# Kernel tuning notes

Measured on AMD Instinct MI355X. Metric: run time of the kernel, lower is better.

The kernel has to match this reference:

```python
import jax, jax.numpy as jnp
import numpy as np

NUM_HEADS = 8
DIM_HEAD_QK = 32
DIM_HEAD_V = 32
BLOCK = 8
HALO = 3
WIN = BLOCK + 2 * HALO  # 14
SCALE = DIM_HEAD_QK ** -0.5


def rel_logits_1d(q, rel_k, permute_mask):
    N, H, W, d = q.shape
    rel_size = rel_k.shape[0]
    win = (rel_size + 1) // 2
    x = jnp.einsum('nhwd,rd->nhwr', q, rel_k)
    x = x.reshape(N * H, W, rel_size)
    x = jnp.pad(x, ((0, 0), (0, 0), (0, 1))).reshape(N * H, -1)
    x = jnp.pad(x, ((0, 0), (0, rel_size - W)))
    x = x.reshape(N * H, W + 1, rel_size)[:, :W, win - 1:]
    x = jnp.broadcast_to(x.reshape(N, H, 1, W, win), (N, H, win, W, win))
    return jnp.transpose(x, permute_mask)


def pos_embed_rel(q, height_rel, width_rel):
    BH, NB, HW, d = q.shape
    qb = q.reshape(-1, BLOCK, BLOCK, d)
    rel_w = rel_logits_1d(qb, width_rel, (0, 1, 3, 2, 4))
    rel_h = rel_logits_1d(jnp.swapaxes(qb, 1, 2), height_rel, (0, 3, 1, 4, 2))
    return (rel_h + rel_w).reshape(BH, NB, HW, WIN * WIN)


def reference(x, q_weight, kv_weight, height_rel, width_rel):
    B, C, H, W = x.shape
    nhb, nwb = H // BLOCK, W // BLOCK
    nb = nhb * nwb
    # 1x1 conv projections
    q = jnp.einsum('bchw,oc->bohw', x, q_weight)
    q = q.reshape(B * NUM_HEADS, DIM_HEAD_QK, nhb, BLOCK, nwb, BLOCK)
    q = jnp.transpose(q, (0, 1, 3, 5, 2, 4)).reshape(B * NUM_HEADS, DIM_HEAD_QK, BLOCK * BLOCK, nb)
    q = jnp.swapaxes(q, 1, 3)  # (BH, nb, BLOCK*BLOCK, dhq)
    kv = jnp.einsum('bchw,oc->bohw', x, kv_weight)
    kv = jnp.pad(kv, ((0, 0), (0, 0), (HALO, HALO), (HALO, HALO)))
    # halo windows: overlapping WINxWIN patches strided by BLOCK
    h_idx = jnp.arange(nhb)[:, None] * BLOCK + jnp.arange(WIN)[None, :]
    w_idx = jnp.arange(nwb)[:, None] * BLOCK + jnp.arange(WIN)[None, :]
    kv = kv[:, :, h_idx, :][:, :, :, :, w_idx]
    kv = jnp.transpose(kv, (0, 1, 2, 4, 3, 5)).reshape(
        B * NUM_HEADS, DIM_HEAD_QK + DIM_HEAD_V, nb, WIN * WIN)
    kv = jnp.transpose(kv, (0, 2, 3, 1))
    k, v = kv[..., :DIM_HEAD_QK], kv[..., DIM_HEAD_QK:]
    attn = jnp.einsum('bnqd,bnkd->bnqk', q, k) * SCALE
    attn = attn + pos_embed_rel(q, height_rel, width_rel)
    attn = jax.nn.softmax(attn, axis=-1)
    out = jnp.einsum('bnqk,bnkd->bnqd', attn, v)
    out = jnp.swapaxes(out, 1, 3)  # (BH, dhv, BLOCK*BLOCK, nb)
    out = out.reshape(-1, BLOCK, BLOCK, nhb, nwb)
    out = jnp.transpose(out, (0, 3, 1, 4, 2)).reshape(B, NUM_HEADS * DIM_HEAD_V, H, W)
    return out


def setup_inputs() -> dict:
    key = jax.random.key(0)
    k1, k2, k3, k4, k5 = jax.random.split(key, 5)
    dim = 256
    std = dim ** -0.5
    x = jax.random.normal(k1, (8, 256, 96, 96), dtype=jnp.float32)
    q_weight = jax.random.normal(k2, (256, 256), dtype=jnp.float32) * std
    kv_weight = jax.random.normal(k3, (512, 256), dtype=jnp.float32) * std
    height_rel = jax.random.normal(k4, (2 * WIN - 1, DIM_HEAD_QK), dtype=jnp.float32) * SCALE
    width_rel = jax.random.normal(k5, (2 * WIN - 1, DIM_HEAD_QK), dtype=jnp.float32) * SCALE
    return {'x': x, 'q_weight': q_weight, 'kv_weight': kv_weight,
            'height_rel': height_rel, 'width_rel': width_rel}
```

## Files before the change

kernel.cpp:

```cpp
#include <hip/hip_runtime.h>
#include <math.h>

#define NPIX 9216
#define SCALE 0.17677669529663687f
#define LOG2E 1.4426950408889634f

typedef __attribute__((ext_vector_type(8))) short bh8;
typedef __attribute__((ext_vector_type(4))) float f4;

__device__ __forceinline__ unsigned short f2bf(float f) {
    unsigned u = __float_as_uint(f);
    u += 0x7fff + ((u >> 16) & 1);
    return (unsigned short)(u >> 16);
}
__device__ __forceinline__ void gload_lds16(const void* g, void* l) {
    __builtin_amdgcn_global_load_lds(
        (const __attribute__((address_space(1))) unsigned int*)g,
        (__attribute__((address_space(3))) unsigned int*)l, 16, 0, 0);
}

__global__ void wconv_kernel(const float* __restrict__ qw, const float* __restrict__ kvw,
                             const float* __restrict__ hrel, const float* __restrict__ wrel,
                             unsigned short* __restrict__ Wb,
                             unsigned short* __restrict__ relb) {
    int bid = blockIdx.x, tid = threadIdx.x;
    if (bid < 768) {
        float v = (bid < 256) ? qw[bid * 256 + tid] : kvw[(bid - 256) * 256 + tid];
        Wb[bid * 256 + tid] = f2bf(v);
    } else {
        int e = (bid - 768) * 256 + tid;
        int half = e >> 10, r = (e >> 5) & 31, d = e & 31;
        float v = 0.0f;
        if (r < 27) v = (half ? wrel : hrel)[r * 32 + d] * LOG2E;
        relb[half * 1024 + r * 32 + d] = f2bf(v);
    }
}

__global__ __launch_bounds__(256) void xtrans_kernel(const float* __restrict__ x,
                                                     unsigned short* __restrict__ xt) {
    int b = blockIdx.z;
    int p0 = blockIdx.x * 128, c0 = blockIdx.y * 128;
    int tid = threadIdx.x;
    __shared__ __align__(16) unsigned short ts[128 * 136];
    const float* xb = x + (size_t)b * 256 * NPIX;
    #pragma unroll
    for (int it = 0; it < 16; ++it) {
        int e = it * 256 + tid;
        int ch = e >> 5, p4 = (e & 31) * 4;
        float4 v = *(const float4*)(xb + (size_t)(c0 + ch) * NPIX + p0 + p4);
        ts[(p4 + 0) * 136 + ch] = f2bf(v.x);
        ts[(p4 + 1) * 136 + ch] = f2bf(v.y);
        ts[(p4 + 2) * 136 + ch] = f2bf(v.z);
        ts[(p4 + 3) * 136 + ch] = f2bf(v.w);
    }
    __syncthreads();
    unsigned short* xtb = xt + (size_t)b * NPIX * 256;
    #pragma unroll
    for (int it = 0; it < 8; ++it) {
        int e = it * 256 + tid;
        int p = e >> 4, ck = (e & 15) * 8;
        *(int4*)(xtb + (size_t)(p0 + p) * 256 + c0 + ck) = *(const int4*)&ts[p * 136 + ck];
    }
}

__global__ __launch_bounds__(256) void proj_kernel(const unsigned short* __restrict__ xt,
                                                   const unsigned short* __restrict__ Wb,
                                                   unsigned short* __restrict__ qb,
                                                   unsigned short* __restrict__ kvb) {
    int flat = blockIdx.x + 72 * (blockIdx.y + 6 * blockIdx.z);
    int w = (flat & 7) * 432 + (flat >> 3);
    int n0 = (w % 6) * 128;
    int m0 = ((w / 6) % 72) * 128;
    int b  = w / 432;
    int tid = threadIdx.x, lane = tid & 63, wave = tid >> 6;
    int ll = lane & 15;
    __shared__ __align__(16) char smem[34816];
    char* As = smem;
    char* Bs = smem + 16384;
    const unsigned short* xtb = xt + (size_t)b * NPIX * 256;

    f4 acc[4][4] = {};
    int wm = (wave & 1) * 64, wn = (wave >> 1) * 64;

    for (int k0 = 0; k0 < 256; k0 += 64) {
        __syncthreads();
        #pragma unroll
        for (int i = 0; i < 4; ++i) {
            int c = wave * 4 + i;
            gload_lds16(xtb + (size_t)(m0 + c * 8 + (lane >> 3)) * 256 + k0 + (lane & 7) * 8,
                        As + c * 1024);
            gload_lds16(Wb + (size_t)(n0 + c * 8 + (lane >> 3)) * 256 + k0 + (lane & 7) * 8,
                        Bs + c * 1024);
        }
        __syncthreads();
        #pragma unroll
        for (int ks = 0; ks < 2; ++ks) {
            bh8 af[4], bf[4];
            #pragma unroll
            for (int i = 0; i < 4; ++i)
                af[i] = *(const bh8*)(As + (wm + i * 16 + ll) * 128 + ks * 64 + (lane >> 4) * 16);
            #pragma unroll
            for (int j = 0; j < 4; ++j)
                bf[j] = *(const bh8*)(Bs + (wn + j * 16 + ll) * 128 + ks * 64 + (lane >> 4) * 16);
            #pragma unroll
            for (int i = 0; i < 4; ++i)
                #pragma unroll
                for (int j = 0; j < 4; ++j)
                    acc[i][j] = __builtin_amdgcn_mfma_f32_16x16x32_bf16(af[i], bf[j], acc[i][j], 0, 0, 0);
        }
    }

    __syncthreads();
    unsigned short* ts = (unsigned short*)smem;
    int q4 = (lane >> 4) * 4;
    #pragma unroll
    for (int i = 0; i < 4; ++i) {
        #pragma unroll
        for (int j = 0; j < 4; ++j) {
            int ch = wn + j * 16 + ll;
            #pragma unroll
            for (int r = 0; r < 4; ++r)
                ts[(wm + i * 16 + q4 + r) * 136 + ch] = f2bf(acc[i][j][r]);
        }
    }
    __syncthreads();
    bool isQ = (n0 < 256);
    #pragma unroll
    for (int it = 0; it < 8; ++it) {
        int e = it * 256 + tid;
        int pixl = e >> 4, ck = (e & 15) * 8;
        int4 v = *(const int4*)&ts[pixl * 136 + ck];
        int pix = m0 + pixl, ch = n0 + ck;
        if (isQ) {
            int head = ch >> 5, d = ch & 31;
            *(int4*)&qb[((size_t)(b * 8 + head) * NPIX + pix) * 32 + d] = v;
        } else {
            int c = ch - 256, head = c >> 6, dv = c & 63;
            *(int4*)&kvb[((size_t)(b * 8 + head) * NPIX + pix) * 64 + dv] = v;
        }
    }
}

__global__ __launch_bounds__(256, 4) void attn_kernel(const unsigned short* __restrict__ qbuf,
                                                      const unsigned short* __restrict__ kvbuf,
                                                      const unsigned short* __restrict__ relb,
                                                      float* __restrict__ out) {
    int flat = blockIdx.x + 144 * blockIdx.y;
    int w = (flat & 7) * 1152 + (flat >> 3);
    int nbid = w % 144, bh = w / 144;
    int b = bh >> 3, head = bh & 7;
    int hb = nbid / 12, wblk = nbid % 12;
    int r0 = hb * 8, c0 = wblk * 8;
    int tid = threadIdx.x, lane = tid & 63, wave = tid >> 6;
    int ll = lane & 15, lq = lane >> 4;
    int m0 = wave * 16;

    __shared__ __align__(16) char smem[32512];
    unsigned short* Vt = (unsigned short*)smem;
    unsigned short* Ks = (unsigned short*)(smem + 14336);
    char* strip = smem + 14336 + wave * 4352;
    float*          RhTw = (float*)strip;
    float*          Rww  = (float*)(strip + 2240);
    unsigned short* Ps   = (unsigned short*)strip;
    float*          smR  = (float*)(smem + 32256);

    const unsigned short* qb  = qbuf  + (size_t)bh * NPIX * 32;
    const unsigned short* kvb = kvbuf + (size_t)bh * NPIX * 64;

    int qp0 = m0 + ll;
    int pixq = (r0 + (qp0 >> 3)) * 96 + c0 + (qp0 & 7);
    bh8 aq = *(const bh8*)&qb[(size_t)pixq * 32 + lq * 8];

    for (int e = tid; e < 896; e += 256) {
        int kp = e >> 2, part = e & 3;
        int a = kp >> 4, b2 = kp & 15;
        int gr = r0 + a - 3, gc = c0 + b2 - 3;
        int4 v = {0, 0, 0, 0};
        if (b2 < 14 && (unsigned)gr < 96u && (unsigned)gc < 96u)
            v = *(const int4*)&kvb[(size_t)(gr * 96 + gc) * 64 + part * 8];
        *(int4*)&Ks[kp * 40 + part * 8] = v;
    }

    #pragma unroll
    for (int it = 0; it < 2; ++it) {
        int e = it * 256 + tid;
        int part = e >> 7, kp2 = e & 127;
        if (kp2 < 112) {
            int a = kp2 >> 3, b2 = (kp2 & 7) * 2;
            int gr = r0 + a - 3, gc = c0 + b2 - 3;
            int4 lo = {0, 0, 0, 0}, hi = {0, 0, 0, 0};
            bool rok = ((kp2 & 7) < 7) && ((unsigned)gr < 96u);
            if (rok && (unsigned)gc < 96u)
                lo = *(const int4*)&kvb[(size_t)(gr * 96 + gc) * 64 + 32 + part * 8];
            if (rok && (unsigned)(gc + 1) < 96u)
                hi = *(const int4*)&kvb[(size_t)(gr * 96 + gc + 1) * 64 + 32 + part * 8];
            int g = kp2 >> 2, kb = b2 & 7;
            const unsigned* lw = (const unsigned*)&lo;
            const unsigned* hw = (const unsigned*)&hi;
            #pragma unroll
            for (int jw = 0; jw < 4; ++jw) {
                unsigned l2 = lw[jw], h2 = hw[jw];
                unsigned v0 = (l2 & 0xffffu) | (h2 << 16);
                unsigned v1 = (l2 >> 16) | (h2 & 0xffff0000u);
                int d0 = part * 8 + jw * 2;
                int s0 = (((jw * 2) & 3) + part) & 3;
                int s1 = (((jw * 2 + 1) & 3) + part) & 3;
                *(unsigned*)&Vt[d0 * 224 + ((g ^ s0) * 8) + kb] = v0;
                *(unsigned*)&Vt[(d0 + 1) * 224 + ((g ^ s1) * 8) + kb] = v1;
            }
        }
    }

    __syncthreads();

    f4 zero4 = {0.f, 0.f, 0.f, 0.f};
    f4 S[14];
    #pragma unroll
    for (int t = 0; t < 14; ++t) {
        bh8 bk = *(const bh8*)&Ks[(t * 16 + ll) * 40 + lq * 8];
        S[t] = __builtin_amdgcn_mfma_f32_16x16x32_bf16(aq, bk, zero4, 0, 0, 0);
    }

    __syncthreads();

    #pragma unroll
    for (int t = 0; t < 2; ++t) {
        int r = t * 16 + ll;
        bh8 hbv = *(const bh8*)&relb[(size_t)r * 32 + lq * 8];
        bh8 wbv = *(const bh8*)&relb[1024 + (size_t)r * 32 + lq * 8];
        f4 ch = __builtin_amdgcn_mfma_f32_16x16x32_bf16(aq, hbv, zero4, 0, 0, 0);
        f4 cw = __builtin_amdgcn_mfma_f32_16x16x32_bf16(aq, wbv, zero4, 0, 0, 0);
        if (r < 28) *(f4*)&RhTw[r * 20 + lq * 4] = ch;
        if (r >= 6 && r < 27) {
            #pragma unroll
            for (int rr = 0; rr < 4; ++rr)
                Rww[(lq * 4 + rr) * 23 + (r - 6)] = cw[rr];
        }
    }

    int row0 = m0 + lq * 4;
    int h = row0 >> 3;
    bool valid = (ll < 14);
    float rw4[4];
    #pragma unroll
    for (int rr = 0; rr < 4; ++rr) {
        int row = row0 + rr;
        rw4[rr] = valid ? Rww[(lq * 4 + rr) * 23 + 7 + ll - (row & 7)] : -INFINITY;
    }
    const float SL = SCALE * LOG2E;
    float sm4[4] = {0.f, 0.f, 0.f, 0.f};
    #pragma unroll
    for (int t = 0; t < 14; ++t) {
        f4 rh = *(const f4*)&RhTw[(13 + t - h) * 20 + lq * 4];
        #pragma unroll
        for (int rr = 0; rr < 4; ++rr) {
            float lg = S[t][rr] * SL + rh[rr] + rw4[rr];
            float p = __builtin_amdgcn_exp2f(lg);
            S[t][rr] = p;
            sm4[rr] += p;
        }
    }
    #pragma unroll
    for (int rr = 0; rr < 4; ++rr) {
        sm4[rr] += __shfl_xor(sm4[rr], 1);
        sm4[rr] += __shfl_xor(sm4[rr], 2);
        sm4[rr] += __shfl_xor(sm4[rr], 4);
        sm4[rr] += __shfl_xor(sm4[rr], 8);
    }
    if (ll == 0) {
        #pragma unroll
        for (int rr = 0; rr < 4; ++rr) smR[row0 + rr] = sm4[rr];
    }

    f4 O[2] = {zero4, zero4};
    #pragma unroll
    for (int c = 0; c < 2; ++c) {
        const int nt = c ? 6 : 8;
        #pragma unroll
        for (int tl = 0; tl < 8; ++tl) {
            if (tl < nt) {
                int t = c * 8 + tl;
                int col = tl * 16 + ll;
                #pragma unroll
                for (int rr = 0; rr < 4; ++rr)
                    Ps[(lq * 4 + rr) * 136 + col] = f2bf(S[t][rr]);
            }
        }
        const int nkt = c ? 3 : 4;
        #pragma unroll
        for (int ktl = 0; ktl < 4; ++ktl) {
            if (ktl < nkt) {
                int kt = c * 4 + ktl;
                bh8 bp = *(const bh8*)&Ps[ll * 136 + ktl * 32 + lq * 8];
                #pragma unroll
                for (int mt = 0; mt < 2; ++mt) {
                    int d = mt * 16 + ll;
                    int s = ((d & 3) + ((d >> 3) & 3)) & 3;
                    bh8 av = *(const bh8*)&Vt[d * 224 + (((kt * 4 + lq) ^ s) * 8)];
                    O[mt] = __builtin_amdgcn_mfma_f32_16x16x32_bf16(av, bp, O[mt], 0, 0, 0);
                }
            }
        }
    }

    int qp = m0 + ll;
    float rs = 1.0f / smR[qp];
    int pix = (r0 + (qp >> 3)) * 96 + c0 + (qp & 7);
    float* ob = out + (size_t)(b * 256 + head * 32) * NPIX;
    #pragma unroll
    for (int mt = 0; mt < 2; ++mt) {
        #pragma unroll
        for (int rr = 0; rr < 4; ++rr) {
            int d = mt * 16 + lq * 4 + rr;
            ob[(size_t)d * NPIX + pix] = O[mt][rr] * rs;
        }
    }
}

extern "C" void kernel_launch(void* const* d_in, const int* in_sizes, int n_in,
                              void* d_out, int out_size, void* d_ws, size_t ws_size,
                              hipStream_t stream) {
    const float* x    = (const float*)d_in[0];
    const float* qw   = (const float*)d_in[1];
    const float* kvw  = (const float*)d_in[2];
    const float* hrel = (const float*)d_in[3];
    const float* wrel = (const float*)d_in[4];
    float* out = (float*)d_out;

    char* ws = (char*)d_ws;
    unsigned short* xt    = (unsigned short*)ws;
    unsigned short* Wb    = (unsigned short*)(ws + 37748736);
    unsigned short* relb  = (unsigned short*)(ws + 38141952);
    unsigned short* qbuf  = (unsigned short*)(ws + 38146048);
    unsigned short* kvbuf = (unsigned short*)(ws + 75894784);

    wconv_kernel<<<dim3(776), 256, 0, stream>>>(qw, kvw, hrel, wrel, Wb, relb);
    xtrans_kernel<<<dim3(72, 2, 8), 256, 0, stream>>>(x, xt);
    proj_kernel<<<dim3(72, 6, 8), 256, 0, stream>>>(xt, Wb, qbuf, kvbuf);
    attn_kernel<<<dim3(144, 64), 256, 0, stream>>>(qbuf, kvbuf, relb, out);
}
```

Before: 258.5 us.

## Fold softmax scale into Q projection, drop LDS staging in proj GEMM, pack P stores

Folds SCALE*LOG2E into the Q projection epilogue and rescales the relative-position tables by 1/SCALE so the attention logits need no per-element multiply. The projection GEMM stops staging tiles through LDS and instead loads MFMA fragments straight from global memory into double-buffered registers, and it gains an occupancy launch bound. The xtrans transpose uses an XOR-swizzled LDS layout in place of padding. The P-matrix store in attention exchanges values between neighbouring lanes and writes packed bf16 pairs with v_cvt_pk_bf16_f32. Pre-scaling Q before bf16 rounding slightly changes numerics, and direct global fragment loads are uncoalesced and rely on cache hits for reuse.

```diff
diff --git a/kernel.cpp b/kernel.cpp
--- a/kernel.cpp
+++ b/kernel.cpp
@@ -4,6 +4,8 @@
 #define NPIX 9216
 #define SCALE 0.17677669529663687f
 #define LOG2E 1.4426950408889634f
+#define PSL   (SCALE * LOG2E)
+#define RINV  5.656854249492381f
 
 typedef __attribute__((ext_vector_type(8))) short bh8;
 typedef __attribute__((ext_vector_type(4))) float f4;
@@ -12,11 +14,6 @@
     unsigned u = __float_as_uint(f);
     u += 0x7fff + ((u >> 16) & 1);
     return (unsigned short)(u >> 16);
-}
-__device__ __forceinline__ void gload_lds16(const void* g, void* l) {
-    __builtin_amdgcn_global_load_lds(
-        (const __attribute__((address_space(1))) unsigned int*)g,
-        (__attribute__((address_space(3))) unsigned int*)l, 16, 0, 0);
 }
 
 __global__ void wconv_kernel(const float* __restrict__ qw, const float* __restrict__ kvw,
@@ -31,7 +28,7 @@
         int e = (bid - 768) * 256 + tid;
         int half = e >> 10, r = (e >> 5) & 31, d = e & 31;
         float v = 0.0f;
-        if (r < 27) v = (half ? wrel : hrel)[r * 32 + d] * LOG2E;
+        if (r < 27) v = (half ? wrel : hrel)[r * 32 + d] * RINV;
         relb[half * 1024 + r * 32 + d] = f2bf(v);
     }
 }
@@ -41,17 +38,19 @@
     int b = blockIdx.z;
     int p0 = blockIdx.x * 128, c0 = blockIdx.y * 128;
     int tid = threadIdx.x;
-    __shared__ __align__(16) unsigned short ts[128 * 136];
+    __shared__ __align__(16) unsigned short ts[128 * 128];
     const float* xb = x + (size_t)b * 256 * NPIX;
     #pragma unroll
     for (int it = 0; it < 16; ++it) {
         int e = it * 256 + tid;
         int ch = e >> 5, p4 = (e & 31) * 4;
         float4 v = *(const float4*)(xb + (size_t)(c0 + ch) * NPIX + p0 + p4);
-        ts[(p4 + 0) * 136 + ch] = f2bf(v.x);
-        ts[(p4 + 1) * 136 + ch] = f2bf(v.y);
-        ts[(p4 + 2) * 136 + ch] = f2bf(v.z);
-        ts[(p4 + 3) * 136 + ch] = f2bf(v.w);
+        int sw = ((p4 >> 3) & 7) << 4;
+        char* tb = (char*)ts;
+        *(unsigned short*)(tb + (((p4 + 0) * 256 + ch * 2) ^ sw)) = f2bf(v.x);
+        *(unsigned short*)(tb + (((p4 + 1) * 256 + ch * 2) ^ sw)) = f2bf(v.y);
+        *(unsigned short*)(tb + (((p4 + 2) * 256 + ch * 2) ^ sw)) = f2bf(v.z);
+        *(unsigned short*)(tb + (((p4 + 3) * 256 + ch * 2) ^ sw)) = f2bf(v.w);
     }
     __syncthreads();
     unsigned short* xtb = xt + (size_t)b * NPIX * 256;
@@ -59,60 +58,72 @@
     for (int it = 0; it < 8; ++it) {
         int e = it * 256 + tid;
         int p = e >> 4, ck = (e & 15) * 8;
-        *(int4*)(xtb + (size_t)(p0 + p) * 256 + c0 + ck) = *(const int4*)&ts[p * 136 + ck];
-    }
-}
-
-__global__ __launch_bounds__(256) void proj_kernel(const unsigned short* __restrict__ xt,
-                                                   const unsigned short* __restrict__ Wb,
-                                                   unsigned short* __restrict__ qb,
-                                                   unsigned short* __restrict__ kvb) {
+        int bo = (p * 256 + ck * 2) ^ (((p >> 3) & 7) << 4);
+        *(int4*)(xtb + (size_t)(p0 + p) * 256 + c0 + ck) = *(const int4*)((char*)ts + bo);
+    }
+}
+
+__global__ __launch_bounds__(256, 4) void proj_kernel(const unsigned short* __restrict__ xt,
+                                                      const unsigned short* __restrict__ Wb,
+                                                      unsigned short* __restrict__ qb,
+                                                      unsigned short* __restrict__ kvb) {
     int flat = blockIdx.x + 72 * (blockIdx.y + 6 * blockIdx.z);
     int w = (flat & 7) * 432 + (flat >> 3);
     int n0 = (w % 6) * 128;
     int m0 = ((w / 6) % 72) * 128;
     int b  = w / 432;
     int tid = threadIdx.x, lane = tid & 63, wave = tid >> 6;
-    int ll = lane & 15;
-    __shared__ __align__(16) char smem[34816];
-    char* As = smem;
-    char* Bs = smem + 16384;
+    int ll = lane & 15, lq = lane >> 4;
+    int wm = (wave & 1) * 64, wn = (wave >> 1) * 64;
+    __shared__ __align__(16) unsigned short ts[128 * 136];
     const unsigned short* xtb = xt + (size_t)b * NPIX * 256;
 
+    const unsigned short* arow[4];
+    const unsigned short* brow[4];
+    #pragma unroll
+    for (int i = 0; i < 4; ++i) arow[i] = xtb + (size_t)(m0 + wm + i * 16 + ll) * 256 + lq * 8;
+    #pragma unroll
+    for (int j = 0; j < 4; ++j) brow[j] = Wb + (size_t)(n0 + wn + j * 16 + ll) * 256 + lq * 8;
+
     f4 acc[4][4] = {};
-    int wm = (wave & 1) * 64, wn = (wave >> 1) * 64;
-
-    for (int k0 = 0; k0 < 256; k0 += 64) {
-        __syncthreads();
-        #pragma unroll
-        for (int i = 0; i < 4; ++i) {
-            int c = wave * 4 + i;
-            gload_lds16(xtb + (size_t)(m0 + c * 8 + (lane >> 3)) * 256 + k0 + (lane & 7) * 8,
-                        As + c * 1024);
-            gload_lds16(Wb + (size_t)(n0 + c * 8 + (lane >> 3)) * 256 + k0 + (lane & 7) * 8,
-                        Bs + c * 1024);
-        }
-        __syncthreads();
-        #pragma unroll
-        for (int ks = 0; ks < 2; ++ks) {
-            bh8 af[4], bf[4];
+    bh8 aA[4], bA[4], aB[4], bB[4];
+    #pragma unroll
+    for (int i = 0; i < 4; ++i) { aA[i] = *(const bh8*)arow[i]; bA[i] = *(const bh8*)brow[i]; }
+
+    #pragma unroll
+    for (int s = 0; s < 8; ++s) {
+        if ((s & 1) == 0) {
+            if (s < 7) {
+                #pragma unroll
+                for (int i = 0; i < 4; ++i) {
+                    aB[i] = *(const bh8*)(arow[i] + (s + 1) * 32);
+                    bB[i] = *(const bh8*)(brow[i] + (s + 1) * 32);
+                }
+            }
             #pragma unroll
             for (int i = 0; i < 4; ++i)
-                af[i] = *(const bh8*)(As + (wm + i * 16 + ll) * 128 + ks * 64 + (lane >> 4) * 16);
-            #pragma unroll
-            for (int j = 0; j < 4; ++j)
-                bf[j] = *(const bh8*)(Bs + (wn + j * 16 + ll) * 128 + ks * 64 + (lane >> 4) * 16);
+                #pragma unroll
+                for (int j = 0; j < 4; ++j)
+                    acc[i][j] = __builtin_amdgcn_mfma_f32_16x16x32_bf16(aA[i], bA[j], acc[i][j], 0, 0, 0);
+        } else {
+            if (s < 7) {
+                #pragma unroll
+                for (int i = 0; i < 4; ++i) {
+                    aA[i] = *(const bh8*)(arow[i] + (s + 1) * 32);
+                    bA[i] = *(const bh8*)(brow[i] + (s + 1) * 32);
+                }
+            }
             #pragma unroll
             for (int i = 0; i < 4; ++i)
                 #pragma unroll
                 for (int j = 0; j < 4; ++j)
-                    acc[i][j] = __builtin_amdgcn_mfma_f32_16x16x32_bf16(af[i], bf[j], acc[i][j], 0, 0, 0);
-        }
-    }
-
-    __syncthreads();
-    unsigned short* ts = (unsigned short*)smem;
-    int q4 = (lane >> 4) * 4;
+                    acc[i][j] = __builtin_amdgcn_mfma_f32_16x16x32_bf16(aB[i], bB[j], acc[i][j], 0, 0, 0);
+        }
+    }
+
+    bool isQ = (n0 < 256);
+    float osc = isQ ? PSL : 1.0f;
+    int q4 = lq * 4;
     #pragma unroll
     for (int i = 0; i < 4; ++i) {
         #pragma unroll
@@ -120,11 +131,10 @@
             int ch = wn + j * 16 + ll;
             #pragma unroll
             for (int r = 0; r < 4; ++r)
-                ts[(wm + i * 16 + q4 + r) * 136 + ch] = f2bf(acc[i][j][r]);
+                ts[(wm + i * 16 + q4 + r) * 136 + ch] = f2bf(acc[i][j][r] * osc);
         }
     }
     __syncthreads();
-    bool isQ = (n0 < 256);
     #pragma unroll
     for (int it = 0; it < 8; ++it) {
         int e = it * 256 + tid;
@@ -247,14 +257,13 @@
         int row = row0 + rr;
         rw4[rr] = valid ? Rww[(lq * 4 + rr) * 23 + 7 + ll - (row & 7)] : -INFINITY;
     }
-    const float SL = SCALE * LOG2E;
     float sm4[4] = {0.f, 0.f, 0.f, 0.f};
     #pragma unroll
     for (int t = 0; t < 14; ++t) {
         f4 rh = *(const f4*)&RhTw[(13 + t - h) * 20 + lq * 4];
         #pragma unroll
         for (int rr = 0; rr < 4; ++rr) {
-            float lg = S[t][rr] * SL + rh[rr] + rw4[rr];
+            float lg = (S[t][rr] + rh[rr]) + rw4[rr];
             float p = __builtin_amdgcn_exp2f(lg);
             S[t][rr] = p;
             sm4[rr] += p;
@@ -272,6 +281,8 @@
         for (int rr = 0; rr < 4; ++rr) smR[row0 + rr] = sm4[rr];
     }
 
+    int sel = ll & 1;
+    int rowA = lq * 4 + sel * 2;
     f4 O[2] = {zero4, zero4};
     #pragma unroll
     for (int c = 0; c < 2; ++c) {
@@ -280,10 +291,17 @@
         for (int tl = 0; tl < 8; ++tl) {
             if (tl < nt) {
                 int t = c * 8 + tl;
-                int col = tl * 16 + ll;
-                #pragma unroll
-                for (int rr = 0; rr < 4; ++rr)
-                    Ps[(lq * 4 + rr) * 136 + col] = f2bf(S[t][rr]);
+                float o0 = S[t][0], o1 = S[t][1], o2 = S[t][2], o3 = S[t][3];
+                float q0 = __shfl_xor(o0, 1), q1 = __shfl_xor(o1, 1);
+                float q2 = __shfl_xor(o2, 1), q3 = __shfl_xor(o3, 1);
+                float lo0 = sel ? q2 : o0, hi0 = sel ? o2 : q0;
+                float lo1 = sel ? q3 : o1, hi1 = sel ? o3 : q1;
+                unsigned w0, w1;
+                asm("v_cvt_pk_bf16_f32 %0, %1, %2" : "=v"(w0) : "v"(lo0), "v"(hi0));
+                asm("v_cvt_pk_bf16_f32 %0, %1, %2" : "=v"(w1) : "v"(lo1), "v"(hi1));
+                int colp = tl * 16 + (ll & ~1);
+                *(unsigned*)&Ps[rowA * 136 + colp]       = w0;
+                *(unsigned*)&Ps[(rowA + 1) * 136 + colp] = w1;
             }
         }
         const int nkt = c ? 3 : 4;
```

Measured after the change: 432.0 us. 67.1% more time.

## Fold softmax scale into projections, swizzle transpose LDS, pack P stores

Applied to the files above, without the earlier changes.

Folds SCALE*LOG2E into the Q projection epilogue and rescales the relative embeddings so their contribution after the Q product matches the old LOG2E scaling. This removes a multiply per logit in the attention softmax loop. The x-transpose kernel replaces its padded LDS tile with an XOR-swizzled layout, and the P-tile write to LDS now exchanges values between lane pairs and uses packed bf16 conversion to issue 32-bit stores instead of 16-bit ones. Pre-scaling Q before rounding to bf16 changes rounding behaviour slightly.

```diff
diff --git a/kernel.cpp b/kernel.cpp
--- a/kernel.cpp
+++ b/kernel.cpp
@@ -4,6 +4,8 @@
 #define NPIX 9216
 #define SCALE 0.17677669529663687f
 #define LOG2E 1.4426950408889634f
+#define PSL   (SCALE * LOG2E)
+#define RINV  5.656854249492381f
 
 typedef __attribute__((ext_vector_type(8))) short bh8;
 typedef __attribute__((ext_vector_type(4))) float f4;
@@ -31,7 +33,7 @@
         int e = (bid - 768) * 256 + tid;
         int half = e >> 10, r = (e >> 5) & 31, d = e & 31;
         float v = 0.0f;
-        if (r < 27) v = (half ? wrel : hrel)[r * 32 + d] * LOG2E;
+        if (r < 27) v = (half ? wrel : hrel)[r * 32 + d] * RINV;
         relb[half * 1024 + r * 32 + d] = f2bf(v);
     }
 }
@@ -41,17 +43,19 @@
     int b = blockIdx.z;
     int p0 = blockIdx.x * 128, c0 = blockIdx.y * 128;
     int tid = threadIdx.x;
-    __shared__ __align__(16) unsigned short ts[128 * 136];
+    __shared__ __align__(16) unsigned short ts[128 * 128];
     const float* xb = x + (size_t)b * 256 * NPIX;
     #pragma unroll
     for (int it = 0; it < 16; ++it) {
         int e = it * 256 + tid;
         int ch = e >> 5, p4 = (e & 31) * 4;
         float4 v = *(const float4*)(xb + (size_t)(c0 + ch) * NPIX + p0 + p4);
-        ts[(p4 + 0) * 136 + ch] = f2bf(v.x);
-        ts[(p4 + 1) * 136 + ch] = f2bf(v.y);
-        ts[(p4 + 2) * 136 + ch] = f2bf(v.z);
-        ts[(p4 + 3) * 136 + ch] = f2bf(v.w);
+        int sw = ((p4 >> 3) & 7) << 4;
+        char* tb = (char*)ts;
+        *(unsigned short*)(tb + (((p4 + 0) * 256 + ch * 2) ^ sw)) = f2bf(v.x);
+        *(unsigned short*)(tb + (((p4 + 1) * 256 + ch * 2) ^ sw)) = f2bf(v.y);
+        *(unsigned short*)(tb + (((p4 + 2) * 256 + ch * 2) ^ sw)) = f2bf(v.z);
+        *(unsigned short*)(tb + (((p4 + 3) * 256 + ch * 2) ^ sw)) = f2bf(v.w);
     }
     __syncthreads();
     unsigned short* xtb = xt + (size_t)b * NPIX * 256;
@@ -59,7 +63,8 @@
     for (int it = 0; it < 8; ++it) {
         int e = it * 256 + tid;
         int p = e >> 4, ck = (e & 15) * 8;
-        *(int4*)(xtb + (size_t)(p0 + p) * 256 + c0 + ck) = *(const int4*)&ts[p * 136 + ck];
+        int bo = (p * 256 + ck * 2) ^ (((p >> 3) & 7) << 4);
+        *(int4*)(xtb + (size_t)(p0 + p) * 256 + c0 + ck) = *(const int4*)((char*)ts + bo);
     }
 }
 
@@ -112,6 +117,8 @@
 
     __syncthreads();
     unsigned short* ts = (unsigned short*)smem;
+    bool isQ = (n0 < 256);
+    float osc = isQ ? PSL : 1.0f;
     int q4 = (lane >> 4) * 4;
     #pragma unroll
     for (int i = 0; i < 4; ++i) {
@@ -120,11 +127,10 @@
             int ch = wn + j * 16 + ll;
             #pragma unroll
             for (int r = 0; r < 4; ++r)
-                ts[(wm + i * 16 + q4 + r) * 136 + ch] = f2bf(acc[i][j][r]);
-        }
-    }
-    __syncthreads();
-    bool isQ = (n0 < 256);
+                ts[(wm + i * 16 + q4 + r) * 136 + ch] = f2bf(acc[i][j][r] * osc);
+        }
+    }
+    __syncthreads();
     #pragma unroll
     for (int it = 0; it < 8; ++it) {
         int e = it * 256 + tid;
@@ -247,14 +253,13 @@
         int row = row0 + rr;
         rw4[rr] = valid ? Rww[(lq * 4 + rr) * 23 + 7 + ll - (row & 7)] : -INFINITY;
     }
-    const float SL = SCALE * LOG2E;
     float sm4[4] = {0.f, 0.f, 0.f, 0.f};
     #pragma unroll
     for (int t = 0; t < 14; ++t) {
         f4 rh = *(const f4*)&RhTw[(13 + t - h) * 20 + lq * 4];
         #pragma unroll
         for (int rr = 0; rr < 4; ++rr) {
-            float lg = S[t][rr] * SL + rh[rr] + rw4[rr];
+            float lg = (S[t][rr] + rh[rr]) + rw4[rr];
             float p = __builtin_amdgcn_exp2f(lg);
             S[t][rr] = p;
             sm4[rr] += p;
@@ -272,6 +277,8 @@
         for (int rr = 0; rr < 4; ++rr) smR[row0 + rr] = sm4[rr];
     }
 
+    int sel = ll & 1;
+    int rowA = lq * 4 + sel * 2;
     f4 O[2] = {zero4, zero4};
     #pragma unroll
     for (int c = 0; c < 2; ++c) {
@@ -280,10 +287,17 @@
         for (int tl = 0; tl < 8; ++tl) {
             if (tl < nt) {
                 int t = c * 8 + tl;
-                int col = tl * 16 + ll;
-                #pragma unroll
-                for (int rr = 0; rr < 4; ++rr)
-                    Ps[(lq * 4 + rr) * 136 + col] = f2bf(S[t][rr]);
+                float o0 = S[t][0], o1 = S[t][1], o2 = S[t][2], o3 = S[t][3];
+                float q0 = __shfl_xor(o0, 1), q1 = __shfl_xor(o1, 1);
+                float q2 = __shfl_xor(o2, 1), q3 = __shfl_xor(o3, 1);
+                float lo0 = sel ? q2 : o0, hi0 = sel ? o2 : q0;
+                float lo1 = sel ? q3 : o1, hi1 = sel ? o3 : q1;
+                unsigned w0, w1;
+                asm("v_cvt_pk_bf16_f32 %0, %1, %2" : "=v"(w0) : "v"(lo0), "v"(hi0));
+                asm("v_cvt_pk_bf16_f32 %0, %1, %2" : "=v"(w1) : "v"(lo1), "v"(hi1));
+                int colp = tl * 16 + (ll & ~1);
+                *(unsigned*)&Ps[rowA * 136 + colp]       = w0;
+                *(unsigned*)&Ps[(rowA + 1) * 136 + colp] = w1;
             }
         }
         const int nkt = c ? 3 : 4;
```

New measurement: 265.9 us. 1.03x slower.
